# Kernel optimization log

Measured on AMD Instinct MI355X. Metric: run time of the kernel, lower is better.

## Reference

```python
import jax, jax.numpy as jnp
import numpy as np
from jax import lax

B, NC, NF = 16, 1024, 4096   # clouds, coarse pts/cloud, fine pts/cloud
C_IN, C_SKIP, C_HID, K = 256, 128, 256, 3
BN_EPS = 1e-5


def setup_inputs() -> dict:
    key = jax.random.key(0)
    ks = jax.random.split(key, 12)
    inp = {
        "x": jax.random.normal(ks[0], (B * NC, C_IN), jnp.float32),
        "pos": jax.random.normal(ks[1], (B * NC, 3), jnp.float32),
        "batch": jnp.arange(B * NC, dtype=jnp.int64) // NC,
        "x_skip": jax.random.normal(ks[2], (B * NF, C_SKIP), jnp.float32),
        "pos_skip": jax.random.normal(ks[3], (B * NF, 3), jnp.float32),
        "batch_skip": jnp.arange(B * NF, dtype=jnp.int64) // NF,
    }
    d_in = C_IN + C_SKIP
    inp["W1"] = jax.random.normal(ks[4], (d_in, C_HID), jnp.float32) / np.sqrt(d_in)
    inp["b1"] = jnp.zeros((C_HID,), jnp.float32)
    inp["g1"] = jnp.ones((C_HID,), jnp.float32)
    inp["be1"] = jnp.zeros((C_HID,), jnp.float32)
    inp["W2"] = jax.random.normal(ks[5], (C_HID, C_HID), jnp.float32) / np.sqrt(C_HID)
    inp["b2"] = jnp.zeros((C_HID,), jnp.float32)
    inp["g2"] = jnp.ones((C_HID,), jnp.float32)
    inp["be2"] = jnp.zeros((C_HID,), jnp.float32)
    return inp


def _knn_interpolate(x, pos, pos_skip):
    # batches are contiguous equal-size -> reshape per cloud
    xb = x.reshape(B, NC, C_IN)
    pc = pos.reshape(B, NC, 3)
    pf = pos_skip.reshape(B, NF, 3)
    # squared distances [B, NF, NC]
    d2 = jnp.sum((pf[:, :, None, :] - pc[:, None, :, :]) ** 2, axis=-1)
    neg_d, idx = lax.top_k(-d2, K)                      # [B, NF, K]
    w = 1.0 / jnp.maximum(-neg_d, 1e-16)                # inverse-squared-distance weights
    feats = xb[jnp.arange(B)[:, None, None], idx]       # [B, NF, K, C_IN]
    out = jnp.sum(w[..., None] * feats, axis=2) / jnp.sum(w, axis=2, keepdims=True)
    return out.reshape(B * NF, C_IN)


def _mlp_layer(h, W, b, g, be):
    z = jax.nn.relu(h @ W + b)
    mean = jnp.mean(z, axis=0)
    var = jnp.mean((z - mean) ** 2, axis=0)            # biased var, as torch BN
    return (z - mean) * lax.rsqrt(var + BN_EPS) * g + be


def reference(x, pos, batch, x_skip, pos_skip, batch_skip,
              W1, b1, g1, be1, W2, b2, g2, be2):
    h = _knn_interpolate(x, pos, pos_skip)
    h = jnp.concatenate([h, x_skip], axis=1)            # [B*NF, C_IN+C_SKIP]
    h = _mlp_layer(h, W1, b1, g1, be1)
    h = _mlp_layer(h, W2, b2, g2, be2)
    return h
```

## Files before the change

kernel.cpp:

```cpp
#include <hip/hip_runtime.h>
#include <hip/hip_bf16.h>

#define NB    16
#define NC    1024
#define NF    4096
#define MROWS 65536
#define CIN   256
#define CSK   128
#define DIN   384
#define CHID  256
#define BN_EPS 1e-5f

typedef __attribute__((ext_vector_type(8))) short bf16x8;
typedef __attribute__((ext_vector_type(4))) float f32x4;

__device__ __forceinline__ unsigned short f2bfu(float f) {
  __hip_bfloat16 h = __float2bfloat16(f);
  return __builtin_bit_cast(unsigned short, h);
}
__device__ __forceinline__ float bfu2f(unsigned short u) {
  unsigned int w = ((unsigned int)u) << 16;
  return __builtin_bit_cast(float, w);
}

__device__ __forceinline__ void load_lds16(const void* g, void* lds) {
  __builtin_amdgcn_global_load_lds(
      (const __attribute__((address_space(1))) unsigned int*)g,
      (__attribute__((address_space(3))) unsigned int*)lds, 16, 0, 0);
}

__global__ __launch_bounds__(512) void knn_interp_kernel(
    const float* __restrict__ x,
    const float* __restrict__ pos,
    const float* __restrict__ x_skip,
    const float* __restrict__ pos_skip,
    __hip_bfloat16* __restrict__ h0,
    const float* __restrict__ W1,
    __hip_bfloat16* __restrict__ W1t,
    float* __restrict__ stats)
{
  const int tid = threadIdx.x, wid = tid >> 6, lane = tid & 63;

  if (blockIdx.x >= 1024) {
    const int c = blockIdx.x - 1024;
    if (c == 0 && tid < 256) {
      for (int k = tid; k < 1024; k += 256) stats[k] = 0.f;
    }
    if (tid < 256)
      W1t[(size_t)tid * DIN + c] = __float2bfloat16(W1[(size_t)c * CHID + tid]);
    return;
  }

  __shared__ float4 cpos[NC];
  __shared__ float  md[8][64][3];
  __shared__ int    mi[8][64][3];
  __shared__ float  fw[64][3];
  __shared__ int    fi[64][3];

  const int f0 = blockIdx.x * 64;
  const int b  = f0 >> 12;

  const float* pb = pos + (size_t)b * NC * 3;
  for (int j = tid; j < NC; j += 512)
    cpos[j] = make_float4(pb[3 * j], pb[3 * j + 1], pb[3 * j + 2], 0.f);
  __syncthreads();

  const int f = f0 + lane;
  const float* pf = pos_skip + (size_t)f * 3;
  const float fx = pf[0], fy = pf[1], fz = pf[2];

  float b0 = 3.4e38f, b1 = 3.4e38f, b2v = 3.4e38f;
  int   i0 = 0, i1 = 0, i2 = 0;
  const int jbase = wid * 128;
#pragma unroll 8
  for (int jj = 0; jj < 128; ++jj) {
    const float4 c = cpos[jbase + jj];
    const float dx = __fsub_rn(fx, c.x);
    const float dy = __fsub_rn(fy, c.y);
    const float dz = __fsub_rn(fz, c.z);
    const float d2 = __fadd_rn(
        __fadd_rn(__fmul_rn(dx, dx), __fmul_rn(dy, dy)), __fmul_rn(dz, dz));
    const int j = jbase + jj;
    const bool c0 = d2 < b0, c1 = d2 < b1, c2 = d2 < b2v;
    const float nb1 = __builtin_amdgcn_fmed3f(d2, b0, b1);
    const float nb2 = __builtin_amdgcn_fmed3f(d2, b1, b2v);
    i2  = c1 ? i1 : (c2 ? j : i2);
    i1  = c0 ? i0 : (c1 ? j : i1);
    i0  = c0 ? j : i0;
    b2v = nb2;
    b1  = nb1;
    b0  = fminf(d2, b0);
  }
  md[wid][lane][0] = b0;  md[wid][lane][1] = b1;  md[wid][lane][2] = b2v;
  mi[wid][lane][0] = i0;  mi[wid][lane][1] = i1;  mi[wid][lane][2] = i2;
  __syncthreads();

  if (wid == 0) {
#pragma unroll
    for (int q = 1; q < 8; ++q) {
#pragma unroll
      for (int e = 0; e < 3; ++e) {
        const float d = md[q][lane][e];
        const int   j = mi[q][lane][e];
        const bool c0 = d < b0, c1 = d < b1, c2 = d < b2v;
        const float nb1 = __builtin_amdgcn_fmed3f(d, b0, b1);
        const float nb2 = __builtin_amdgcn_fmed3f(d, b1, b2v);
        i2  = c1 ? i1 : (c2 ? j : i2);
        i1  = c0 ? i0 : (c1 ? j : i1);
        i0  = c0 ? j : i0;
        b2v = nb2;
        b1  = nb1;
        b0  = fminf(d, b0);
      }
    }
    float w0 = 1.f / fmaxf(b0, 1e-16f);
    float w1 = 1.f / fmaxf(b1, 1e-16f);
    float w2 = 1.f / fmaxf(b2v, 1e-16f);
    const float inv = 1.f / (w0 + w1 + w2);
    fw[lane][0] = w0 * inv; fw[lane][1] = w1 * inv; fw[lane][2] = w2 * inv;
    fi[lane][0] = i0; fi[lane][1] = i1; fi[lane][2] = i2;
  }
  __syncthreads();

  for (int pp = 0; pp < 8; ++pp) {
    const int p = wid * 8 + pp;
    const float w0 = fw[p][0], w1 = fw[p][1], w2 = fw[p][2];
    const int j0 = fi[p][0], j1 = fi[p][1], j2 = fi[p][2];
    const float4* r0 = (const float4*)(x + (size_t)(b * NC + j0) * CIN);
    const float4* r1 = (const float4*)(x + (size_t)(b * NC + j1) * CIN);
    const float4* r2 = (const float4*)(x + (size_t)(b * NC + j2) * CIN);
    const float4 a0 = r0[lane], a1 = r1[lane], a2 = r2[lane];
    float4 v;
    v.x = w0 * a0.x + w1 * a1.x + w2 * a2.x;
    v.y = w0 * a0.y + w1 * a1.y + w2 * a2.y;
    v.z = w0 * a0.z + w1 * a1.z + w2 * a2.z;
    v.w = w0 * a0.w + w1 * a1.w + w2 * a2.w;
    __hip_bfloat16* orow = h0 + (size_t)(f0 + p) * DIN;
    ushort4 o;
    o.x = f2bfu(v.x); o.y = f2bfu(v.y); o.z = f2bfu(v.z); o.w = f2bfu(v.w);
    ((ushort4*)orow)[lane] = o;
    const float2 s = ((const float2*)(x_skip + (size_t)(f0 + p) * CSK))[lane];
    const unsigned int packed =
        ((unsigned int)f2bfu(s.y) << 16) | (unsigned int)f2bfu(s.x);
    ((unsigned int*)(orow + CIN))[lane] = packed;
  }
}

__global__ __launch_bounds__(256) void prep_w2b2_kernel(
    const float* __restrict__ W2, const float* __restrict__ stats,
    const float* __restrict__ g1, const float* __restrict__ be1,
    const float* __restrict__ b2, __hip_bfloat16* __restrict__ W2t,
    float* __restrict__ b2p) {
  const int n = blockIdx.x, c = threadIdx.x;
  const int wid = c >> 6, lane = c & 63;
  const float m = stats[c] * (1.f / MROWS);
  const float var = stats[256 + c] * (1.f / MROWS) - m * m;
  const float sc = g1[c] * rsqrtf(var + BN_EPS);
  const float sh = be1[c] - m * sc;
  const float w = W2[(size_t)c * CHID + n];
  W2t[(size_t)n * CHID + c] = __float2bfloat16(sc * w);
  float p = sh * w;
#pragma unroll
  for (int off = 32; off > 0; off >>= 1) p += __shfl_down(p, off);
  __shared__ float red4[4];
  if (lane == 0) red4[wid] = p;
  __syncthreads();
  if (c == 0) b2p[n] = red4[0] + red4[1] + red4[2] + red4[3] + b2[n];
}

template<int KD>
__global__ __launch_bounds__(512) void gemm_bias_relu(
    const __hip_bfloat16* __restrict__ A,
    const __hip_bfloat16* __restrict__ Bt,
    const float* __restrict__ bias,
    __hip_bfloat16* __restrict__ out,
    float* __restrict__ gsum,
    float* __restrict__ gsq)
{
  __shared__ __hip_bfloat16 As[128 * 32];
  __shared__ __hip_bfloat16 Bs[256 * 32];
  __shared__ float ssum[256], ssq[256];
  const int tid = threadIdx.x;
  const int wid = tid >> 6, lane = tid & 63;
  const int bm = blockIdx.x;
  const int wr = wid >> 2, wc = wid & 3;
  const int la = lane & 15, lk = lane >> 4;

  if (tid < 256) { ssum[tid] = 0.f; ssq[tid] = 0.f; }

  f32x4 acc[4][4] = {};

  const int rA = tid >> 2;
  const int c8 = (tid & 3) * 8;
  const __hip_bfloat16* gA  = A  + (size_t)(bm * 128 + rA) * KD + c8;
  const __hip_bfloat16* gB0 = Bt + (size_t)rA * KD + c8;
  const __hip_bfloat16* gB1 = Bt + (size_t)(128 + rA) * KD + c8;
  char* ldsA  = (char*)As + wid * 1024;
  char* ldsB0 = (char*)Bs + wid * 1024;
  char* ldsB1 = (char*)Bs + 8192 + wid * 1024;

  const int nIter = KD / 32;
  for (int it = 0; it < nIter; ++it) {
    const int k0 = it * 32;
    load_lds16(gA  + k0, ldsA);
    load_lds16(gB0 + k0, ldsB0);
    load_lds16(gB1 + k0, ldsB1);
    __syncthreads();

    bf16x8 af[4], bfr[4];
#pragma unroll
    for (int m = 0; m < 4; ++m)
      af[m] = *(const bf16x8*)(As + (wr * 64 + m * 16 + la) * 32 + lk * 8);
#pragma unroll
    for (int n = 0; n < 4; ++n)
      bfr[n] = *(const bf16x8*)(Bs + (wc * 64 + n * 16 + la) * 32 + lk * 8);
#pragma unroll
    for (int m = 0; m < 4; ++m)
#pragma unroll
      for (int n = 0; n < 4; ++n)
        acc[m][n] = __builtin_amdgcn_mfma_f32_16x16x32_bf16(
            af[m], bfr[n], acc[m][n], 0, 0, 0);
    __syncthreads();
  }

  const int rowBase = bm * 128 + wr * 64 + lk * 4;
#pragma unroll
  for (int n = 0; n < 4; ++n) {
    const int col = wc * 64 + n * 16 + la;
    const float bs = bias[col];
    float ls = 0.f, ls2 = 0.f;
#pragma unroll
    for (int m = 0; m < 4; ++m) {
      const int row = rowBase + m * 16;
#pragma unroll
      for (int j = 0; j < 4; ++j) {
        float v = acc[m][n][j] + bs;
        v = fmaxf(v, 0.f);
        ls += v; ls2 += v * v;
        out[(size_t)(row + j) * 256 + col] = __float2bfloat16(v);
      }
    }
    atomicAdd(&ssum[col], ls);
    atomicAdd(&ssq[col], ls2);
  }
  __syncthreads();
  if (tid < 256) {
    atomicAdd(&gsum[tid], ssum[tid]);
    atomicAdd(&gsq[tid], ssq[tid]);
  }
}

__global__ __launch_bounds__(256) void bn_apply_kernel(
    const __hip_bfloat16* __restrict__ Z, const float* __restrict__ stats,
    const float* __restrict__ g2, const float* __restrict__ be2,
    float* __restrict__ out) {
  __shared__ float ssc[256], ssh[256];
  const int t = threadIdx.x;
  {
    const float m = stats[t] * (1.f / MROWS);
    const float var = stats[256 + t] * (1.f / MROWS) - m * m;
    const float sc = g2[t] * rsqrtf(var + BN_EPS);
    ssc[t] = sc;
    ssh[t] = be2[t] - m * sc;
  }
  __syncthreads();
  const size_t i8 = (size_t)blockIdx.x * 256 + t;
  const uint4 raw = ((const uint4*)Z)[i8];
  const int c0 = (int)((i8 * 8) & 255);
  const float4 scA = *(const float4*)(ssc + c0);
  const float4 scB = *(const float4*)(ssc + c0 + 4);
  const float4 shA = *(const float4*)(ssh + c0);
  const float4 shB = *(const float4*)(ssh + c0 + 4);
  float4 oa, ob;
  oa.x = bfu2f((unsigned short)(raw.x & 0xffff)) * scA.x + shA.x;
  oa.y = bfu2f((unsigned short)(raw.x >> 16))    * scA.y + shA.y;
  oa.z = bfu2f((unsigned short)(raw.y & 0xffff)) * scA.z + shA.z;
  oa.w = bfu2f((unsigned short)(raw.y >> 16))    * scA.w + shA.w;
  ob.x = bfu2f((unsigned short)(raw.z & 0xffff)) * scB.x + shB.x;
  ob.y = bfu2f((unsigned short)(raw.z >> 16))    * scB.y + shB.y;
  ob.z = bfu2f((unsigned short)(raw.w & 0xffff)) * scB.z + shB.z;
  ob.w = bfu2f((unsigned short)(raw.w >> 16))    * scB.w + shB.w;
  ((float4*)(out))[i8 * 2]     = oa;
  ((float4*)(out))[i8 * 2 + 1] = ob;
}

extern "C" void kernel_launch(void* const* d_in, const int* in_sizes, int n_in,
                              void* d_out, int out_size, void* d_ws,
                              size_t ws_size, hipStream_t stream) {
  (void)in_sizes; (void)n_in; (void)out_size; (void)ws_size;
  const float* x        = (const float*)d_in[0];
  const float* pos      = (const float*)d_in[1];
  const float* x_skip   = (const float*)d_in[3];
  const float* pos_skip = (const float*)d_in[4];
  const float* W1  = (const float*)d_in[6];
  const float* b1  = (const float*)d_in[7];
  const float* g1  = (const float*)d_in[8];
  const float* be1 = (const float*)d_in[9];
  const float* W2  = (const float*)d_in[10];
  const float* b2  = (const float*)d_in[11];
  const float* g2  = (const float*)d_in[12];
  const float* be2 = (const float*)d_in[13];
  float* out = (float*)d_out;

  char* ws = (char*)d_ws;
  __hip_bfloat16* h0  = (__hip_bfloat16*)(ws);
  __hip_bfloat16* z2  = (__hip_bfloat16*)(ws);
  __hip_bfloat16* W1t = (__hip_bfloat16*)(ws + 50331648);
  __hip_bfloat16* z1  = (__hip_bfloat16*)(ws + 50528256);
  __hip_bfloat16* W2t = (__hip_bfloat16*)(ws + 84082688);
  float* b2p    = (float*)(ws + 84213760);
  float* stats  = (float*)(ws + 84214784);

  knn_interp_kernel<<<1408, 512, 0, stream>>>(x, pos, x_skip, pos_skip, h0,
                                              W1, W1t, stats);
  gemm_bias_relu<DIN><<<512, 512, 0, stream>>>(h0, W1t, b1, z1,
                                               stats, stats + 256);
  prep_w2b2_kernel<<<256, 256, 0, stream>>>(W2, stats, g1, be1, b2, W2t, b2p);
  gemm_bias_relu<CHID><<<512, 512, 0, stream>>>(z1, W2t, b2p, z2,
                                                stats + 512, stats + 768);
  bn_apply_kernel<<<8192, 256, 0, stream>>>(z2, stats + 512, g2, be2, out);
}
```

Before: 142.9 us.

## Double-buffer GEMM LDS tiles and pack KNN distance math into float pairs

The GEMM kernel now uses two LDS buffers for its A and B tiles. The next K-slice is loaded with async global-to-LDS copies while MFMAs run on the current slice, which removes one barrier per iteration and hides load latency, at the cost of twice the LDS. The KNN kernel stores negated coarse positions as pairs (xy packed as f32x4, z as f32x2). It then computes two squared distances per iteration with vector ops that can map to packed-FP32 instructions, with contraction disabled to keep rounding identical. The top-3 insertion is factored into a helper; processing order and tie behaviour stay the same.

```diff
diff --git a/kernel.cpp b/kernel.cpp
--- a/kernel.cpp
+++ b/kernel.cpp
@@ -13,6 +13,7 @@
 
 typedef __attribute__((ext_vector_type(8))) short bf16x8;
 typedef __attribute__((ext_vector_type(4))) float f32x4;
+typedef __attribute__((ext_vector_type(2))) float f32x2;
 
 __device__ __forceinline__ unsigned short f2bfu(float f) {
   __hip_bfloat16 h = __float2bfloat16(f);
@@ -27,6 +28,19 @@
   __builtin_amdgcn_global_load_lds(
       (const __attribute__((address_space(1))) unsigned int*)g,
       (__attribute__((address_space(3))) unsigned int*)lds, 16, 0, 0);
+}
+
+__device__ __forceinline__ void ins3(float d2, int j, float& b0, float& b1,
+                                     float& b2v, int& i0, int& i1, int& i2) {
+  const bool c0 = d2 < b0, c1 = d2 < b1, c2 = d2 < b2v;
+  const float nb1 = __builtin_amdgcn_fmed3f(d2, b0, b1);
+  const float nb2 = __builtin_amdgcn_fmed3f(d2, b1, b2v);
+  i2  = c1 ? i1 : (c2 ? j : i2);
+  i1  = c0 ? i0 : (c1 ? j : i1);
+  i0  = c0 ? j : i0;
+  b2v = nb2;
+  b1  = nb1;
+  b0  = fminf(d2, b0);
 }
 
 __global__ __launch_bounds__(512) void knn_interp_kernel(
@@ -51,7 +65,8 @@
     return;
   }
 
-  __shared__ float4 cpos[NC];
+  __shared__ f32x4 nxy[512];
+  __shared__ f32x2 nz[512];
   __shared__ float  md[8][64][3];
   __shared__ int    mi[8][64][3];
   __shared__ float  fw[64][3];
@@ -61,35 +76,38 @@
   const int b  = f0 >> 12;
 
   const float* pb = pos + (size_t)b * NC * 3;
-  for (int j = tid; j < NC; j += 512)
-    cpos[j] = make_float4(pb[3 * j], pb[3 * j + 1], pb[3 * j + 2], 0.f);
+  for (int j = tid; j < 512; j += 512) {
+    const float* p = pb + 6 * j;
+    nxy[j] = (f32x4){-p[0], -p[3], -p[1], -p[4]};
+    nz[j]  = (f32x2){-p[2], -p[5]};
+  }
   __syncthreads();
 
   const int f = f0 + lane;
   const float* pf = pos_skip + (size_t)f * 3;
   const float fx = pf[0], fy = pf[1], fz = pf[2];
+  const f32x4 fxxyy = (f32x4){fx, fx, fy, fy};
+  const f32x2 fzz = (f32x2){fz, fz};
 
   float b0 = 3.4e38f, b1 = 3.4e38f, b2v = 3.4e38f;
   int   i0 = 0, i1 = 0, i2 = 0;
-  const int jbase = wid * 128;
-#pragma unroll 8
-  for (int jj = 0; jj < 128; ++jj) {
-    const float4 c = cpos[jbase + jj];
-    const float dx = __fsub_rn(fx, c.x);
-    const float dy = __fsub_rn(fy, c.y);
-    const float dz = __fsub_rn(fz, c.z);
-    const float d2 = __fadd_rn(
-        __fadd_rn(__fmul_rn(dx, dx), __fmul_rn(dy, dy)), __fmul_rn(dz, dz));
-    const int j = jbase + jj;
-    const bool c0 = d2 < b0, c1 = d2 < b1, c2 = d2 < b2v;
-    const float nb1 = __builtin_amdgcn_fmed3f(d2, b0, b1);
-    const float nb2 = __builtin_amdgcn_fmed3f(d2, b1, b2v);
-    i2  = c1 ? i1 : (c2 ? j : i2);
-    i1  = c0 ? i0 : (c1 ? j : i1);
-    i0  = c0 ? j : i0;
-    b2v = nb2;
-    b1  = nb1;
-    b0  = fminf(d2, b0);
+  const int pbase = wid * 64;
+#pragma unroll 4
+  for (int p = 0; p < 64; ++p) {
+    const f32x4 cxy = nxy[pbase + p];
+    const f32x2 cz  = nz[pbase + p];
+    f32x2 d2;
+    {
+#pragma clang fp contract(off)
+      const f32x4 dxy = fxxyy + cxy;
+      const f32x4 sq  = dxy * dxy;
+      const f32x2 sxy = (f32x2){sq[0], sq[1]} + (f32x2){sq[2], sq[3]};
+      const f32x2 dz  = fzz + cz;
+      d2 = sxy + dz * dz;
+    }
+    const int j = 2 * (pbase + p);
+    ins3(d2[0], j,     b0, b1, b2v, i0, i1, i2);
+    ins3(d2[1], j + 1, b0, b1, b2v, i0, i1, i2);
   }
   md[wid][lane][0] = b0;  md[wid][lane][1] = b1;  md[wid][lane][2] = b2v;
   mi[wid][lane][0] = i0;  mi[wid][lane][1] = i1;  mi[wid][lane][2] = i2;
@@ -97,22 +115,11 @@
 
   if (wid == 0) {
 #pragma unroll
-    for (int q = 1; q < 8; ++q) {
-#pragma unroll
-      for (int e = 0; e < 3; ++e) {
-        const float d = md[q][lane][e];
-        const int   j = mi[q][lane][e];
-        const bool c0 = d < b0, c1 = d < b1, c2 = d < b2v;
-        const float nb1 = __builtin_amdgcn_fmed3f(d, b0, b1);
-        const float nb2 = __builtin_amdgcn_fmed3f(d, b1, b2v);
-        i2  = c1 ? i1 : (c2 ? j : i2);
-        i1  = c0 ? i0 : (c1 ? j : i1);
-        i0  = c0 ? j : i0;
-        b2v = nb2;
-        b1  = nb1;
-        b0  = fminf(d, b0);
-      }
-    }
+    for (int q = 1; q < 8; ++q)
+#pragma unroll
+      for (int e = 0; e < 3; ++e)
+        ins3(md[q][lane][e], mi[q][lane][e], b0, b1, b2v, i0, i1, i2);
+
     float w0 = 1.f / fmaxf(b0, 1e-16f);
     float w1 = 1.f / fmaxf(b1, 1e-16f);
     float w2 = 1.f / fmaxf(b2v, 1e-16f);
@@ -177,8 +184,8 @@
     float* __restrict__ gsum,
     float* __restrict__ gsq)
 {
-  __shared__ __hip_bfloat16 As[128 * 32];
-  __shared__ __hip_bfloat16 Bs[256 * 32];
+  __shared__ __hip_bfloat16 As[2 * 128 * 32];
+  __shared__ __hip_bfloat16 Bs[2 * 256 * 32];
   __shared__ float ssum[256], ssq[256];
   const int tid = threadIdx.x;
   const int wid = tid >> 6, lane = tid & 63;
@@ -197,23 +204,30 @@
   const __hip_bfloat16* gB1 = Bt + (size_t)(128 + rA) * KD + c8;
   char* ldsA  = (char*)As + wid * 1024;
   char* ldsB0 = (char*)Bs + wid * 1024;
-  char* ldsB1 = (char*)Bs + 8192 + wid * 1024;
+
+  load_lds16(gA,       ldsA);
+  load_lds16(gB0,      ldsB0);
+  load_lds16(gB1,      ldsB0 + 8192);
+  __syncthreads();
 
   const int nIter = KD / 32;
   for (int it = 0; it < nIter; ++it) {
-    const int k0 = it * 32;
-    load_lds16(gA  + k0, ldsA);
-    load_lds16(gB0 + k0, ldsB0);
-    load_lds16(gB1 + k0, ldsB1);
-    __syncthreads();
-
+    const int cur = it & 1, nxt = cur ^ 1;
+    if (it + 1 < nIter) {
+      const int k1 = (it + 1) * 32;
+      load_lds16(gA  + k1, ldsA  + nxt * 8192);
+      load_lds16(gB0 + k1, ldsB0 + nxt * 16384);
+      load_lds16(gB1 + k1, ldsB0 + nxt * 16384 + 8192);
+    }
+    const __hip_bfloat16* Acur = As + cur * 4096;
+    const __hip_bfloat16* Bcur = Bs + cur * 8192;
     bf16x8 af[4], bfr[4];
 #pragma unroll
     for (int m = 0; m < 4; ++m)
-      af[m] = *(const bf16x8*)(As + (wr * 64 + m * 16 + la) * 32 + lk * 8);
+      af[m] = *(const bf16x8*)(Acur + (wr * 64 + m * 16 + la) * 32 + lk * 8);
 #pragma unroll
     for (int n = 0; n < 4; ++n)
-      bfr[n] = *(const bf16x8*)(Bs + (wc * 64 + n * 16 + la) * 32 + lk * 8);
+      bfr[n] = *(const bf16x8*)(Bcur + (wc * 64 + n * 16 + la) * 32 + lk * 8);
 #pragma unroll
     for (int m = 0; m < 4; ++m)
 #pragma unroll
```

Result: faster. 136.9 us (-4.2%).
